# Kernel optimization log

Hardware: AMD Instinct MI355X
Metric: run time of the kernel (lower is better)

## Reference

```python
import jax, jax.numpy as jnp
import numpy as np

B, N, F = 2, 2048, 256
H = 8
O = F // H  # nhid = 32
L = 3       # stacked GraphAttentionLayers
ALPHA = 0.2
NEG = jnp.float32(-1e15)


def setup_inputs() -> dict:
    key = jax.random.key(0)
    ks = jax.random.split(key, 6)
    x = jax.random.normal(ks[0], (B, N, F), dtype=jnp.float32)
    adj = jax.random.randint(ks[1], (B, N, N), 0, 2, dtype=jnp.int32)
    # per-layer multi-head params: W [L,H,F,O], a [L,H,2O]
    W_heads = jax.random.normal(ks[2], (L, H, F, O), dtype=jnp.float32) * 0.1
    a_heads = jax.random.normal(ks[3], (L, H, 2 * O), dtype=jnp.float32) * 0.1
    # per-layer out_att params (single head, F->F)
    W_out = jax.random.normal(ks[4], (L, F, F), dtype=jnp.float32) * 0.05
    a_out = jax.random.normal(ks[5], (L, 2 * F), dtype=jnp.float32) * 0.05
    return {"x": x, "adj": adj, "W_heads": W_heads, "a_heads": a_heads,
            "W_out": W_out, "a_out": a_out}


def _gat_heads(h, mask, W, a1, a2):
    """h: [B,N,F], mask: [B,N,N] bool, W: [H,F,O], a1/a2: [H,O] -> [B,H,N,O]."""
    Wh = jnp.einsum('bnf,hfo->bhno', h, W)
    s1 = jnp.einsum('bhno,ho->bhn', Wh, a1)   # a[:O] projection
    s2 = jnp.einsum('bhno,ho->bhn', Wh, a2)   # a[O:] projection
    e = s1[:, :, :, None] + s2[:, :, None, :]  # additive score [B,H,N,N]
    e = jnp.where(e > 0, e, ALPHA * e)         # LeakyReLU(alpha)
    e = jnp.where(mask[:, None, :, :], e, NEG)
    att = jax.nn.softmax(e, axis=-1)           # dropout is identity in eval
    hp = jnp.einsum('bhnm,bhmo->bhno', att, Wh)
    return jax.nn.elu(hp)                      # activate_function inside head


def reference(x, adj, W_heads, a_heads, W_out, a_out):
    mask = adj > 0
    h = x
    for l in range(L):
        a1 = a_heads[l, :, :O]
        a2 = a_heads[l, :, O:]
        hh = _gat_heads(h, mask, W_heads[l], a1, a2)      # [B,H,N,O]
        h = jnp.transpose(hh, (0, 2, 1, 3)).reshape(B, N, F)  # concat heads
        ao1 = a_out[l, :F][None]
        ao2 = a_out[l, F:][None]
        ho = _gat_heads(h, mask, W_out[l][None], ao1, ao2)[:, 0]  # [B,N,F]
        h = jax.nn.elu(ho)  # extra F.elu in GraphAttentionLayer (elu twice)
    return h
```

## Files before the change

### kernel.cpp

```cpp
#include <hip/hip_runtime.h>
#include <math.h>

#if __has_builtin(__builtin_amdgcn_exp2f)
#define EXP2(x) __builtin_amdgcn_exp2f(x)
#else
#define EXP2(x) exp2f(x)
#endif

#define ALPHA_LRELU 0.2f
#define LOG2E 1.4426950408889634f
#define ESHIFT 6.0f
#define BIGM 1024.0f

constexpr int Bc = 2, Nn = 2048, Ff = 256, Hh = 8, Oo = 32;

typedef _Float16 f16;
typedef f16 f16x8 __attribute__((ext_vector_type(8)));
typedef f16 f16x4 __attribute__((ext_vector_type(4)));
typedef float f32x4 __attribute__((ext_vector_type(4)));
typedef unsigned long long u64;
typedef unsigned u32;

__global__ __launch_bounds__(256) void zero_kernel(float* __restrict__ p) {
    p[blockIdx.x * 256 + threadIdx.x] = 0.f;
}

__global__ __launch_bounds__(256) void pack_kernel(
    const int* __restrict__ adj, u32* __restrict__ maskT) {
    int idx = blockIdx.x * 256 + threadIdx.x;
    u64 bl = __ballot(adj[idx] != 0);
    int lane = threadIdx.x & 63;
    int i = (idx >> 11) & 2047;
    int b = idx >> 22;
    int j0 = (idx & 2047) & ~63;
    int c32 = j0 >> 5;
    if (lane == 0)
        maskT[((size_t)b * 64 + c32) * 2048 + i] = (u32)bl;
    else if (lane == 1)
        maskT[((size_t)b * 64 + c32 + 1) * 2048 + i] = (u32)(bl >> 32);
}

__global__ __launch_bounds__(256) void wt_kernel(
    const float* __restrict__ W_heads, const float* __restrict__ W_out,
    f16* __restrict__ WTF) {
    int t = threadIdx.x;
    int y = blockIdx.y;
    int l = y >> 1, st = y & 1;
    int col = blockIdx.x * 4 + (t >> 6);
    int k0 = (t & 63) * 4;
    const float* src;
    int stride;
    if (st == 0) {
        src = W_heads + (((size_t)l * Hh + (col >> 5)) * Ff) * Oo + (col & 31);
        stride = Oo;
    } else {
        src = W_out + (size_t)l * Ff * Ff + col;
        stride = Ff;
    }
    f16x4 v;
#pragma unroll
    for (int i = 0; i < 4; ++i) v[i] = (f16)src[(size_t)(k0 + i) * stride];
    int cg = col >> 4, am = col & 15;
    int c = k0 >> 5, aq = (k0 >> 3) & 3, i0 = k0 & 7;
    WTF += (((size_t)y * 16 + cg) * 8 + c) * 512 + (aq * 16 + am) * 8 + i0;
    *(f16x4*)WTF = v;
}

__global__ __launch_bounds__(256) void apack_kernel(
    const float* __restrict__ A, f16* __restrict__ Af) {
    int t = threadIdx.x;
    int lane = t & 63;
    int slot = blockIdx.x * 4 + (t >> 6);
    int am = lane & 15, aq = lane >> 4;
    int mt = slot >> 3, c = slot & 7;
    const float* ap = A + ((size_t)mt * 16 + am) * Ff + c * 32 + aq * 8;
    f32x4 v0 = *(const f32x4*)ap;
    f32x4 v1 = *(const f32x4*)(ap + 4);
    f16x8 o;
#pragma unroll
    for (int i = 0; i < 4; ++i) { o[i] = (f16)v0[i]; o[4 + i] = (f16)v1[i]; }
    *(f16x8*)&Af[(size_t)slot * 512 + lane * 8] = o;
}

__global__ __launch_bounds__(256) void gemm_wave(
    const f16* __restrict__ Af, const f16* __restrict__ WTF,
    const float* __restrict__ pa, f16* __restrict__ WhFrag,
    float* __restrict__ s1, float* __restrict__ s2,
    int G, int Ofull, int oshift) {
    int t = threadIdx.x;
    int w = t >> 6, lane = t & 63;
    int am = lane & 15, aq = lane >> 4;
    int mt = blockIdx.x * 4 + w;
    int colb = blockIdx.y * 16;

    const f16* ap = Af + (size_t)(mt * 8) * 512 + lane * 8;
    const f16* bp = WTF + (size_t)((colb >> 4) * 8) * 512 + lane * 8;

    f32x4 acc = {0.f, 0.f, 0.f, 0.f};
    f16x8 a0 = *(const f16x8*)ap;
    f16x8 b0 = *(const f16x8*)bp;
#pragma unroll
    for (int c = 0; c < 8; ++c) {
        int cn = (c + 1 < 8) ? c + 1 : 0;
        f16x8 an = *(const f16x8*)(ap + cn * 512);
        f16x8 bn = *(const f16x8*)(bp + cn * 512);
        acc = __builtin_amdgcn_mfma_f32_16x16x32_f16(a0, b0, acc, 0, 0, 0);
        a0 = an; b0 = bn;
    }

    int m0 = mt * 16;
    int b = m0 >> 11;
    int nn0 = (m0 & 2047) + aq * 4;
    int cO = (m0 & 2047) >> 5;
    int aq_p = ((mt & 1) << 1) | (aq >> 1);
    int i0p = (aq & 1) << 2;
    int g = colb >> oshift;
    size_t bg = (size_t)b * G + g;
    int cg = (colb & (Ofull - 1)) >> 4;

    f16x4 c4;
#pragma unroll
    for (int e = 0; e < 4; ++e) c4[e] = (f16)acc[e];
    *(f16x4*)&WhFrag[(((bg * (Ofull >> 4) + cg) * 64 + cO) * 512) +
                     (aq_p * 16 + am) * 8 + i0p] = c4;

    int o0 = (colb & (Ofull - 1)) + am;
    const float* a1p = pa + 2 * (size_t)g * Ofull;
    float a10 = a1p[o0];
    float a20 = a1p[Ofull + o0];
#pragma unroll
    for (int e = 0; e < 4; ++e) {
        float p1 = acc[e] * a10;
        float p2 = acc[e] * a20;
#pragma unroll
        for (int s = 1; s < 16; s <<= 1) {
            p1 += __shfl_xor(p1, s);
            p2 += __shfl_xor(p2, s);
        }
        if (am == 0) {
            size_t sidx = bg * Nn + nn0 + e;
            atomicAdd(&s1[sidx], p1);
            atomicAdd(&s2[sidx], p2);
        }
    }
}

template <bool OUT, bool FINAL>
__global__ __launch_bounds__(256) void attn_kernel(
    const f16* __restrict__ WhFrag, const float* __restrict__ s1,
    const float* __restrict__ s2, const u32* __restrict__ maskT,
    float* __restrict__ dst, f16* __restrict__ AfOut) {
    constexpr float C0 = -ESHIFT * LOG2E - BIGM;
    constexpr int NCG = OUT ? 16 : 2;
    constexpr int TSTR = 40;
    __shared__ float Ls[4][64];
    __shared__ float As[4][64][8];
    __shared__ f16 T[2][16 * TSTR];

    int t = threadIdx.x;
    int w = t >> 6, lane = t & 63;
    int am = lane & 15, aq = lane >> 4;
    int wr = w & 1;
    int wh = w >> 1;
    int i0 = blockIdx.x * 32 + wr * 16;
    int bz = blockIdx.z;
    int b = OUT ? bz : (bz >> 3);
    int cg0 = OUT ? blockIdx.y * 2 : 0;
    int dstcol = OUT ? cg0 * 16 : (bz & 7) * Oo;

    const f16* bp0 = WhFrag + ((size_t)bz * NCG + cg0) * 64 * 512 + lane * 8;
    const f16* bp1 = bp0 + 64 * 512;
    const float* s2p = s2 + (size_t)bz * Nn + aq * 8;
    float s1v = s1[(size_t)bz * Nn + i0 + am];
    const u32* mtp = maskT + (size_t)b * 64 * 2048 + i0 + am;

    f32x4 acc0 = {0.f, 0.f, 0.f, 0.f}, acc1 = acc0;
    float lacc = 0.f;

    int cbeg = wh * 32, cend = cbeg + 32;

    f16x8 xb0, xb1, yb0, yb1;
    f32x4 xv0, xv1, yv0, yv1;
    u32 xm, ym;
    auto ld = [&](int c, f16x8& b0, f16x8& b1, f32x4& v0, f32x4& v1, u32& m) {
        b0 = *(const f16x8*)(bp0 + c * 512);
        b1 = *(const f16x8*)(bp1 + c * 512);
        v0 = *(const f32x4*)(s2p + c * 32);
        v1 = *(const f32x4*)(s2p + c * 32 + 4);
        m = mtp[c * 2048];
    };
    auto comp = [&](f16x8 b0, f16x8 b1, f32x4 v0, f32x4 v1, u32 m) {
        u32 bits = (m >> (aq * 8)) & 0xffu;
        f16x8 af;
#pragma unroll
        for (int k = 0; k < 8; ++k) {
            float xv = s1v + (k < 4 ? v0[k] : v1[k - 4]);
            float lr = fmaxf(xv, ALPHA_LRELU * xv);
            float bitf = (float)((bits >> k) & 1u);
            float p = EXP2(fmaf(bitf, BIGM, fmaf(lr, LOG2E, C0)));
            lacc += p;
            af[k] = (f16)p;
        }
        acc0 = __builtin_amdgcn_mfma_f32_16x16x32_f16(af, b0, acc0, 0, 0, 0);
        acc1 = __builtin_amdgcn_mfma_f32_16x16x32_f16(af, b1, acc1, 0, 0, 0);
    };

    ld(cbeg, xb0, xb1, xv0, xv1, xm);
    ld(cbeg + 1, yb0, yb1, yv0, yv1, ym);
    for (int c = cbeg; c < cend; c += 2) {
        comp(xb0, xb1, xv0, xv1, xm);
        ld(c + 2 < cend ? c + 2 : cbeg, xb0, xb1, xv0, xv1, xm);
        comp(yb0, yb1, yv0, yv1, ym);
        ld(c + 3 < cend ? c + 3 : cbeg, yb0, yb1, yv0, yv1, ym);
    }

    lacc += __shfl_xor(lacc, 16);
    lacc += __shfl_xor(lacc, 32);

    Ls[w][lane] = lacc;
#pragma unroll
    for (int e = 0; e < 4; ++e) {
        As[w][lane][e] = acc0[e];
        As[w][lane][4 + e] = acc1[e];
    }
    __syncthreads();

    if (wh == 0) {
        float lt = Ls[w][lane] + Ls[w + 2][lane];
        f32x4 a0, a1;
#pragma unroll
        for (int e = 0; e < 4; ++e) {
            a0[e] = As[w][lane][e] + As[w + 2][lane][e];
            a1[e] = As[w][lane][4 + e] + As[w + 2][lane][4 + e];
        }
        f16* Tw = T[wr];
#pragma unroll
        for (int e = 0; e < 4; ++e) {
            int r = aq * 4 + e;
            float li = __shfl(lt, r);
            float v0 = a0[e] / li, v1 = a1[e] / li;
            v0 = v0 > 0.f ? v0 : __expf(v0) - 1.f;
            v1 = v1 > 0.f ? v1 : __expf(v1) - 1.f;
            if (OUT) {
                v0 = v0 > 0.f ? v0 : __expf(v0) - 1.f;
                v1 = v1 > 0.f ? v1 : __expf(v1) - 1.f;
            }
            if (FINAL) {
                size_t base = ((size_t)b * Nn + i0 + r) * Ff + dstcol;
                dst[base + am] = v0;
                dst[base + 16 + am] = v1;
            } else {
                Tw[r * TSTR + am] = (f16)v0;
                Tw[r * TSTR + 16 + am] = (f16)v1;
            }
        }
        if (!FINAL) {
            f16x8 o = *(const f16x8*)&Tw[am * TSTR + aq * 8];
            int mt = (b * Nn + i0) >> 4;
            int c = dstcol >> 5;
            *(f16x8*)&AfOut[(size_t)(mt * 8 + c) * 512 + lane * 8] = o;
        }
    }
}

extern "C" void kernel_launch(void* const* d_in, const int* in_sizes, int n_in,
                              void* d_out, int out_size, void* d_ws, size_t ws_size,
                              hipStream_t stream) {
    const float* x = (const float*)d_in[0];
    const int* adj = (const int*)d_in[1];
    const float* W_heads = (const float*)d_in[2];
    const float* a_heads = (const float*)d_in[3];
    const float* W_out = (const float*)d_in[4];
    const float* a_out = (const float*)d_in[5];
    float* out = (float*)d_out;

    float* ws = (float*)d_ws;
    const size_t M = (size_t)Bc * Nn * Ff;
    f16* Af_a = (f16*)ws;
    f16* Af_b = (f16*)(ws + M / 2);
    f16* WhFrag = (f16*)(ws + M);
    u32* maskT = (u32*)(ws + 3 * M / 2);
    f16* WTF = (f16*)(ws + 3 * M / 2 + M / 4);
    float* sbuf = ws + 3 * M / 2 + M / 4 + 196608;
    const size_t SH = (size_t)Bc * Hh * Nn;
    const size_t SO = (size_t)Bc * Nn;
    const size_t SL = 2 * SH + 2 * SO;

    zero_kernel<<<(3 * SL) / 256, 256, 0, stream>>>(sbuf);
    pack_kernel<<<(Bc * Nn * Nn) / 256, 256, 0, stream>>>(adj, maskT);
    wt_kernel<<<dim3(Ff / 4, 6), 256, 0, stream>>>(W_heads, W_out, WTF);
    apack_kernel<<<(Bc * Nn * Ff / 8) / 256, 256, 0, stream>>>(x, Af_a);

    for (int l = 0; l < 3; ++l) {
        float* s1h = sbuf + l * SL;
        float* s2h = s1h + SH;
        float* s1o = s2h + SH;
        float* s2o = s1o + SO;

        gemm_wave<<<dim3((Bc * Nn) / 64, Ff / 16), 256, 0, stream>>>(
            Af_a, WTF + (size_t)(2 * l) * Ff * Ff,
            a_heads + (size_t)l * Hh * 2 * Oo, WhFrag, s1h, s2h, Hh, Oo, 5);
        attn_kernel<false, false><<<dim3(Nn / 32, 1, Bc * Hh), 256, 0, stream>>>(
            WhFrag, s1h, s2h, maskT, nullptr, Af_b);

        gemm_wave<<<dim3((Bc * Nn) / 64, Ff / 16), 256, 0, stream>>>(
            Af_b, WTF + (size_t)(2 * l + 1) * Ff * Ff,
            a_out + (size_t)l * 2 * Ff, WhFrag, s1o, s2o, 1, Ff, 8);
        if (l == 2) {
            attn_kernel<true, true><<<dim3(Nn / 32, Ff / 32, Bc), 256, 0, stream>>>(
                WhFrag, s1o, s2o, maskT, out, nullptr);
        } else {
            attn_kernel<true, false><<<dim3(Nn / 32, Ff / 32, Bc), 256, 0, stream>>>(
                WhFrag, s1o, s2o, maskT, nullptr, Af_a);
        }
    }
}
```

Before: 301.7 us.

## Fuse all stages into one persistent kernel with hierarchical grid barriers

Replaces the sequence of about sixteen kernel launches (zeroing, packing, GEMMs, attention per layer) with one persistent mega-kernel of 1024 blocks. Stages are separated by a two-level atomic grid barrier, and a small init kernel zeroes the score buffers and barrier counters. The aim is to remove launch overhead and inter-kernel gaps. The risks are deadlock if all 1024 blocks cannot be co-resident (launch_bounds 256,4 is meant to allow this), spin-wait cost at each barrier, and added register pressure in the fused kernel.

```diff
diff --git a/kernel.cpp b/kernel.cpp
--- a/kernel.cpp
+++ b/kernel.cpp
@@ -13,6 +13,7 @@
 #define BIGM 1024.0f
 
 constexpr int Bc = 2, Nn = 2048, Ff = 256, Hh = 8, Oo = 32;
+constexpr int NBLK = 1024;
 
 typedef _Float16 f16;
 typedef f16 f16x8 __attribute__((ext_vector_type(8)));
@@ -21,77 +22,42 @@
 typedef unsigned long long u64;
 typedef unsigned u32;
 
-__global__ __launch_bounds__(256) void zero_kernel(float* __restrict__ p) {
-    p[blockIdx.x * 256 + threadIdx.x] = 0.f;
-}
-
-__global__ __launch_bounds__(256) void pack_kernel(
-    const int* __restrict__ adj, u32* __restrict__ maskT) {
-    int idx = blockIdx.x * 256 + threadIdx.x;
-    u64 bl = __ballot(adj[idx] != 0);
-    int lane = threadIdx.x & 63;
-    int i = (idx >> 11) & 2047;
-    int b = idx >> 22;
-    int j0 = (idx & 2047) & ~63;
-    int c32 = j0 >> 5;
-    if (lane == 0)
-        maskT[((size_t)b * 64 + c32) * 2048 + i] = (u32)bl;
-    else if (lane == 1)
-        maskT[((size_t)b * 64 + c32 + 1) * 2048 + i] = (u32)(bl >> 32);
-}
-
-__global__ __launch_bounds__(256) void wt_kernel(
-    const float* __restrict__ W_heads, const float* __restrict__ W_out,
-    f16* __restrict__ WTF) {
-    int t = threadIdx.x;
-    int y = blockIdx.y;
-    int l = y >> 1, st = y & 1;
-    int col = blockIdx.x * 4 + (t >> 6);
-    int k0 = (t & 63) * 4;
-    const float* src;
-    int stride;
-    if (st == 0) {
-        src = W_heads + (((size_t)l * Hh + (col >> 5)) * Ff) * Oo + (col & 31);
-        stride = Oo;
-    } else {
-        src = W_out + (size_t)l * Ff * Ff + col;
-        stride = Ff;
-    }
-    f16x4 v;
-#pragma unroll
-    for (int i = 0; i < 4; ++i) v[i] = (f16)src[(size_t)(k0 + i) * stride];
-    int cg = col >> 4, am = col & 15;
-    int c = k0 >> 5, aq = (k0 >> 3) & 3, i0 = k0 & 7;
-    WTF += (((size_t)y * 16 + cg) * 8 + c) * 512 + (aq * 16 + am) * 8 + i0;
-    *(f16x4*)WTF = v;
-}
-
-__global__ __launch_bounds__(256) void apack_kernel(
-    const float* __restrict__ A, f16* __restrict__ Af) {
-    int t = threadIdx.x;
-    int lane = t & 63;
-    int slot = blockIdx.x * 4 + (t >> 6);
-    int am = lane & 15, aq = lane >> 4;
-    int mt = slot >> 3, c = slot & 7;
-    const float* ap = A + ((size_t)mt * 16 + am) * Ff + c * 32 + aq * 8;
-    f32x4 v0 = *(const f32x4*)ap;
-    f32x4 v1 = *(const f32x4*)(ap + 4);
-    f16x8 o;
-#pragma unroll
-    for (int i = 0; i < 4; ++i) { o[i] = (f16)v0[i]; o[4 + i] = (f16)v1[i]; }
-    *(f16x8*)&Af[(size_t)slot * 512 + lane * 8] = o;
-}
-
-__global__ __launch_bounds__(256) void gemm_wave(
+__global__ __launch_bounds__(256) void init_kernel(float* __restrict__ sbuf,
+                                                   u32* __restrict__ bar) {
+    int g = blockIdx.x * 256 + threadIdx.x;
+    if (g < 544) bar[g] = 0;
+    if (g < 221184) sbuf[g] = 0.f;
+}
+
+__device__ __forceinline__ void gridbar(u32* bar, int ph) {
+    __syncthreads();
+    if (threadIdx.x == 0) {
+        __threadfence();
+        u32* lv1 = bar + 32 + (blockIdx.x & 15) * 32;
+        u32 old = __hip_atomic_fetch_add(lv1, 1u, __ATOMIC_RELAXED,
+                                         __HIP_MEMORY_SCOPE_AGENT);
+        if (old == (u32)(ph * 64 + 63))
+            __hip_atomic_fetch_add(bar, 1u, __ATOMIC_RELAXED,
+                                   __HIP_MEMORY_SCOPE_AGENT);
+        while (__hip_atomic_load(bar, __ATOMIC_RELAXED,
+                                 __HIP_MEMORY_SCOPE_AGENT) <
+               (u32)(ph * 16 + 16))
+            __builtin_amdgcn_s_sleep(2);
+        __threadfence();
+    }
+    __syncthreads();
+}
+
+__device__ __forceinline__ void gemm_phase(
     const f16* __restrict__ Af, const f16* __restrict__ WTF,
     const float* __restrict__ pa, f16* __restrict__ WhFrag,
     float* __restrict__ s1, float* __restrict__ s2,
-    int G, int Ofull, int oshift) {
+    int G, int Ofull, int oshift, int xb, int yb) {
     int t = threadIdx.x;
     int w = t >> 6, lane = t & 63;
     int am = lane & 15, aq = lane >> 4;
-    int mt = blockIdx.x * 4 + w;
-    int colb = blockIdx.y * 16;
+    int mt = xb * 4 + w;
+    int colb = yb * 16;
 
     const f16* ap = Af + (size_t)(mt * 8) * 512 + lane * 8;
     const f16* bp = WTF + (size_t)((colb >> 4) * 8) * 512 + lane * 8;
@@ -146,26 +112,24 @@
 }
 
 template <bool OUT, bool FINAL>
-__global__ __launch_bounds__(256) void attn_kernel(
+__device__ __forceinline__ void attn_phase(
     const f16* __restrict__ WhFrag, const float* __restrict__ s1,
     const float* __restrict__ s2, const u32* __restrict__ maskT,
-    float* __restrict__ dst, f16* __restrict__ AfOut) {
+    float* __restrict__ dst, f16* __restrict__ AfOut,
+    int xb, int yb, int bz,
+    float (&Ls)[4][64], float (&As)[4][64][8], f16 (&T)[2][640]) {
     constexpr float C0 = -ESHIFT * LOG2E - BIGM;
     constexpr int NCG = OUT ? 16 : 2;
     constexpr int TSTR = 40;
-    __shared__ float Ls[4][64];
-    __shared__ float As[4][64][8];
-    __shared__ f16 T[2][16 * TSTR];
 
     int t = threadIdx.x;
     int w = t >> 6, lane = t & 63;
     int am = lane & 15, aq = lane >> 4;
     int wr = w & 1;
     int wh = w >> 1;
-    int i0 = blockIdx.x * 32 + wr * 16;
-    int bz = blockIdx.z;
+    int i0 = xb * 32 + wr * 16;
     int b = OUT ? bz : (bz >> 3);
-    int cg0 = OUT ? blockIdx.y * 2 : 0;
+    int cg0 = OUT ? yb * 2 : 0;
     int dstcol = OUT ? cg0 * 16 : (bz & 7) * Oo;
 
     const f16* bp0 = WhFrag + ((size_t)bz * NCG + cg0) * 64 * 512 + lane * 8;
@@ -263,6 +227,109 @@
     }
 }
 
+__global__ __launch_bounds__(256, 4) void mega_kernel(
+    const int* __restrict__ adj, const float* __restrict__ x,
+    const float* __restrict__ W_heads, const float* __restrict__ a_heads,
+    const float* __restrict__ W_out, const float* __restrict__ a_out,
+    float* __restrict__ out, f16* __restrict__ Af_a, f16* __restrict__ Af_b,
+    f16* __restrict__ WhFrag, u32* __restrict__ maskT, f16* __restrict__ WTF,
+    float* __restrict__ sbuf, u32* __restrict__ bar) {
+    __shared__ float Ls[4][64];
+    __shared__ float As[4][64][8];
+    __shared__ f16 T[2][640];
+
+    const int B = blockIdx.x;
+    const int t = threadIdx.x;
+    int ph = 0;
+
+    if (B < 768) {
+        for (int idx = B * 256 + t; idx < Bc * Nn * Nn; idx += 768 * 256) {
+            u64 bl = __ballot(adj[idx] != 0);
+            int lane = t & 63;
+            int i = (idx >> 11) & 2047;
+            int b = idx >> 22;
+            int c32 = ((idx & 2047) & ~63) >> 5;
+            if (lane == 0)
+                maskT[((size_t)b * 64 + c32) * 2048 + i] = (u32)bl;
+            else if (lane == 1)
+                maskT[((size_t)b * 64 + c32 + 1) * 2048 + i] = (u32)(bl >> 32);
+        }
+    } else if (B < 896) {
+        int w = t >> 6, lane = t & 63;
+        int am = lane & 15, aq = lane >> 4;
+#pragma unroll
+        for (int it = 0; it < 4; ++it) {
+            int slot = (B - 768) * 4 + w + it * 512;
+            int mt = slot >> 3, c = slot & 7;
+            const float* ap = x + ((size_t)mt * 16 + am) * Ff + c * 32 + aq * 8;
+            f32x4 v0 = *(const f32x4*)ap;
+            f32x4 v1 = *(const f32x4*)(ap + 4);
+            f16x8 o;
+#pragma unroll
+            for (int i = 0; i < 4; ++i) { o[i] = (f16)v0[i]; o[4 + i] = (f16)v1[i]; }
+            *(f16x8*)&Af_a[(size_t)slot * 512 + lane * 8] = o;
+        }
+    } else {
+#pragma unroll
+        for (int it = 0; it < 3; ++it) {
+            int unit = (B - 896) * 3 + it;
+            int y = unit >> 6, bx = unit & 63;
+            int ll = y >> 1, st = y & 1;
+            int col = bx * 4 + (t >> 6);
+            int k0 = (t & 63) * 4;
+            const float* src;
+            int stride;
+            if (st == 0) {
+                src = W_heads + (((size_t)ll * Hh + (col >> 5)) * Ff) * Oo + (col & 31);
+                stride = Oo;
+            } else {
+                src = W_out + (size_t)ll * Ff * Ff + col;
+                stride = Ff;
+            }
+            f16x4 v;
+#pragma unroll
+            for (int i = 0; i < 4; ++i) v[i] = (f16)src[(size_t)(k0 + i) * stride];
+            int cg = col >> 4, am = col & 15;
+            int c = k0 >> 5, aq = (k0 >> 3) & 3, i0 = k0 & 7;
+            *(f16x4*)&WTF[(((size_t)y * 16 + cg) * 8 + c) * 512 +
+                          (aq * 16 + am) * 8 + i0] = v;
+        }
+    }
+    gridbar(bar, ph++);
+
+    const size_t SH = (size_t)Bc * Hh * Nn;
+    const size_t SO = (size_t)Bc * Nn;
+    const size_t SL = 2 * SH + 2 * SO;
+
+    for (int l = 0; l < 3; ++l) {
+        float* s1h = sbuf + l * SL;
+        float* s2h = s1h + SH;
+        float* s1o = s2h + SH;
+        float* s2o = s1o + SO;
+
+        gemm_phase(Af_a, WTF + (size_t)(2 * l) * Ff * Ff,
+                   a_heads + (size_t)l * Hh * 2 * Oo, WhFrag, s1h, s2h,
+                   Hh, Oo, 5, B & 63, B >> 6);
+        gridbar(bar, ph++);
+        attn_phase<false, false>(WhFrag, s1h, s2h, maskT, nullptr, Af_b,
+                                 B & 63, 0, B >> 6, Ls, As, T);
+        gridbar(bar, ph++);
+
+        gemm_phase(Af_b, WTF + (size_t)(2 * l + 1) * Ff * Ff,
+                   a_out + (size_t)l * 2 * Ff, WhFrag, s1o, s2o,
+                   1, Ff, 8, B & 63, B >> 6);
+        gridbar(bar, ph++);
+        if (l == 2) {
+            attn_phase<true, true>(WhFrag, s1o, s2o, maskT, out, nullptr,
+                                   B & 63, (B >> 6) & 7, B >> 9, Ls, As, T);
+        } else {
+            attn_phase<true, false>(WhFrag, s1o, s2o, maskT, nullptr, Af_a,
+                                    B & 63, (B >> 6) & 7, B >> 9, Ls, As, T);
+            gridbar(bar, ph++);
+        }
+    }
+}
+
 extern "C" void kernel_launch(void* const* d_in, const int* in_sizes, int n_in,
                               void* d_out, int out_size, void* d_ws, size_t ws_size,
                               hipStream_t stream) {
@@ -282,36 +349,10 @@
     u32* maskT = (u32*)(ws + 3 * M / 2);
     f16* WTF = (f16*)(ws + 3 * M / 2 + M / 4);
     float* sbuf = ws + 3 * M / 2 + M / 4 + 196608;
-    const size_t SH = (size_t)Bc * Hh * Nn;
-    const size_t SO = (size_t)Bc * Nn;
-    const size_t SL = 2 * SH + 2 * SO;
-
-    zero_kernel<<<(3 * SL) / 256, 256, 0, stream>>>(sbuf);
-    pack_kernel<<<(Bc * Nn * Nn) / 256, 256, 0, stream>>>(adj, maskT);
-    wt_kernel<<<dim3(Ff / 4, 6), 256, 0, stream>>>(W_heads, W_out, WTF);
-    apack_kernel<<<(Bc * Nn * Ff / 8) / 256, 256, 0, stream>>>(x, Af_a);
-
-    for (int l = 0; l < 3; ++l) {
-        float* s1h = sbuf + l * SL;
-        float* s2h = s1h + SH;
-        float* s1o = s2h + SH;
-        float* s2o = s1o + SO;
-
-        gemm_wave<<<dim3((Bc * Nn) / 64, Ff / 16), 256, 0, stream>>>(
-            Af_a, WTF + (size_t)(2 * l) * Ff * Ff,
-            a_heads + (size_t)l * Hh * 2 * Oo, WhFrag, s1h, s2h, Hh, Oo, 5);
-        attn_kernel<false, false><<<dim3(Nn / 32, 1, Bc * Hh), 256, 0, stream>>>(
-            WhFrag, s1h, s2h, maskT, nullptr, Af_b);
-
-        gemm_wave<<<dim3((Bc * Nn) / 64, Ff / 16), 256, 0, stream>>>(
-            Af_b, WTF + (size_t)(2 * l + 1) * Ff * Ff,
-            a_out + (size_t)l * 2 * Ff, WhFrag, s1o, s2o, 1, Ff, 8);
-        if (l == 2) {
-            attn_kernel<true, true><<<dim3(Nn / 32, Ff / 32, Bc), 256, 0, stream>>>(
-                WhFrag, s1o, s2o, maskT, out, nullptr);
-        } else {
-            attn_kernel<true, false><<<dim3(Nn / 32, Ff / 32, Bc), 256, 0, stream>>>(
-                WhFrag, s1o, s2o, maskT, nullptr, Af_a);
-        }
-    }
-}
+    u32* bar = (u32*)(sbuf + 221184);
+
+    init_kernel<<<NBLK, 256, 0, stream>>>(sbuf, bar);
+    mega_kernel<<<NBLK, 256, 0, stream>>>(
+        adj, x, W_heads, a_heads, W_out, a_out, out,
+        Af_a, Af_b, WhFrag, maskT, WTF, sbuf, bar);
+}
```

Measured after the change: 762.5 us. 2.53x slower.

## Merge prep kernels into one launch and give each attention wave two row tiles

Applied to the files above, without the earlier changes.

The four setup kernels (zeroing, mask bit-packing, weight transpose, input packing) become one prep kernel that splits its blocks by role, cutting launch overhead. In the attention kernel each wave now handles both 16-row tiles over a quarter of the column range, so each loaded Wh fragment and s2 vector feeds four MFMAs instead of two. The cross-wave reduction now sums four partials through larger shared arrays. This adds register pressure and shared memory use.

```diff
diff --git a/kernel.cpp b/kernel.cpp
--- a/kernel.cpp
+++ b/kernel.cpp
@@ -21,65 +21,69 @@
 typedef unsigned long long u64;
 typedef unsigned u32;
 
-__global__ __launch_bounds__(256) void zero_kernel(float* __restrict__ p) {
-    p[blockIdx.x * 256 + threadIdx.x] = 0.f;
-}
-
-__global__ __launch_bounds__(256) void pack_kernel(
-    const int* __restrict__ adj, u32* __restrict__ maskT) {
-    int idx = blockIdx.x * 256 + threadIdx.x;
-    u64 bl = __ballot(adj[idx] != 0);
-    int lane = threadIdx.x & 63;
-    int i = (idx >> 11) & 2047;
-    int b = idx >> 22;
-    int j0 = (idx & 2047) & ~63;
-    int c32 = j0 >> 5;
-    if (lane == 0)
-        maskT[((size_t)b * 64 + c32) * 2048 + i] = (u32)bl;
-    else if (lane == 1)
-        maskT[((size_t)b * 64 + c32 + 1) * 2048 + i] = (u32)(bl >> 32);
-}
-
-__global__ __launch_bounds__(256) void wt_kernel(
+__global__ __launch_bounds__(256) void prep_kernel(
+    const int* __restrict__ adj, const float* __restrict__ x,
     const float* __restrict__ W_heads, const float* __restrict__ W_out,
-    f16* __restrict__ WTF) {
-    int t = threadIdx.x;
-    int y = blockIdx.y;
-    int l = y >> 1, st = y & 1;
-    int col = blockIdx.x * 4 + (t >> 6);
-    int k0 = (t & 63) * 4;
-    const float* src;
-    int stride;
-    if (st == 0) {
-        src = W_heads + (((size_t)l * Hh + (col >> 5)) * Ff) * Oo + (col & 31);
-        stride = Oo;
+    u32* __restrict__ maskT, f16* __restrict__ Af, f16* __restrict__ WTF,
+    float* __restrict__ sbuf) {
+    const int B = blockIdx.x;
+    const int t = threadIdx.x;
+    int g = B * 256 + t;
+    if (g < 221184) sbuf[g] = 0.f;
+
+    if (B < 768) {
+        for (int idx = g; idx < Bc * Nn * Nn; idx += 768 * 256) {
+            u64 bl = __ballot(adj[idx] != 0);
+            int lane = t & 63;
+            int i = (idx >> 11) & 2047;
+            int b = idx >> 22;
+            int c32 = ((idx & 2047) & ~63) >> 5;
+            if (lane == 0)
+                maskT[((size_t)b * 64 + c32) * 2048 + i] = (u32)bl;
+            else if (lane == 1)
+                maskT[((size_t)b * 64 + c32 + 1) * 2048 + i] = (u32)(bl >> 32);
+        }
+    } else if (B < 896) {
+        int w = t >> 6, lane = t & 63;
+        int am = lane & 15, aq = lane >> 4;
+#pragma unroll
+        for (int it = 0; it < 4; ++it) {
+            int slot = (B - 768) * 4 + w + it * 512;
+            int mt = slot >> 3, c = slot & 7;
+            const float* ap = x + ((size_t)mt * 16 + am) * Ff + c * 32 + aq * 8;
+            f32x4 v0 = *(const f32x4*)ap;
+            f32x4 v1 = *(const f32x4*)(ap + 4);
+            f16x8 o;
+#pragma unroll
+            for (int i = 0; i < 4; ++i) { o[i] = (f16)v0[i]; o[4 + i] = (f16)v1[i]; }
+            *(f16x8*)&Af[(size_t)slot * 512 + lane * 8] = o;
+        }
     } else {
-        src = W_out + (size_t)l * Ff * Ff + col;
-        stride = Ff;
-    }
-    f16x4 v;
-#pragma unroll
-    for (int i = 0; i < 4; ++i) v[i] = (f16)src[(size_t)(k0 + i) * stride];
-    int cg = col >> 4, am = col & 15;
-    int c = k0 >> 5, aq = (k0 >> 3) & 3, i0 = k0 & 7;
-    WTF += (((size_t)y * 16 + cg) * 8 + c) * 512 + (aq * 16 + am) * 8 + i0;
-    *(f16x4*)WTF = v;
-}
-
-__global__ __launch_bounds__(256) void apack_kernel(
-    const float* __restrict__ A, f16* __restrict__ Af) {
-    int t = threadIdx.x;
-    int lane = t & 63;
-    int slot = blockIdx.x * 4 + (t >> 6);
-    int am = lane & 15, aq = lane >> 4;
-    int mt = slot >> 3, c = slot & 7;
-    const float* ap = A + ((size_t)mt * 16 + am) * Ff + c * 32 + aq * 8;
-    f32x4 v0 = *(const f32x4*)ap;
-    f32x4 v1 = *(const f32x4*)(ap + 4);
-    f16x8 o;
-#pragma unroll
-    for (int i = 0; i < 4; ++i) { o[i] = (f16)v0[i]; o[4 + i] = (f16)v1[i]; }
-    *(f16x8*)&Af[(size_t)slot * 512 + lane * 8] = o;
+#pragma unroll
+        for (int it = 0; it < 3; ++it) {
+            int unit = (B - 896) * 3 + it;
+            int y = unit >> 6, bx = unit & 63;
+            int ll = y >> 1, st = y & 1;
+            int col = bx * 4 + (t >> 6);
+            int k0 = (t & 63) * 4;
+            const float* src;
+            int stride;
+            if (st == 0) {
+                src = W_heads + (((size_t)ll * Hh + (col >> 5)) * Ff) * Oo + (col & 31);
+                stride = Oo;
+            } else {
+                src = W_out + (size_t)ll * Ff * Ff + col;
+                stride = Ff;
+            }
+            f16x4 v;
+#pragma unroll
+            for (int i = 0; i < 4; ++i) v[i] = (f16)src[(size_t)(k0 + i) * stride];
+            int cg = col >> 4, am = col & 15;
+            int c = k0 >> 5, aq = (k0 >> 3) & 3, i0 = k0 & 7;
+            *(f16x4*)&WTF[(((size_t)y * 16 + cg) * 8 + c) * 512 +
+                          (aq * 16 + am) * 8 + i0] = v;
+        }
+    }
 }
 
 __global__ __launch_bounds__(256) void gemm_wave(
@@ -153,16 +157,14 @@
     constexpr float C0 = -ESHIFT * LOG2E - BIGM;
     constexpr int NCG = OUT ? 16 : 2;
     constexpr int TSTR = 40;
-    __shared__ float Ls[4][64];
-    __shared__ float As[4][64][8];
+    __shared__ float Ls[4][2][64];
+    __shared__ float As[4][64][16];
     __shared__ f16 T[2][16 * TSTR];
 
     int t = threadIdx.x;
     int w = t >> 6, lane = t & 63;
     int am = lane & 15, aq = lane >> 4;
-    int wr = w & 1;
-    int wh = w >> 1;
-    int i0 = blockIdx.x * 32 + wr * 16;
+    int i0 = blockIdx.x * 32;
     int bz = blockIdx.z;
     int b = OUT ? bz : (bz >> 3);
     int cg0 = OUT ? blockIdx.y * 2 : 0;
@@ -171,69 +173,90 @@
     const f16* bp0 = WhFrag + ((size_t)bz * NCG + cg0) * 64 * 512 + lane * 8;
     const f16* bp1 = bp0 + 64 * 512;
     const float* s2p = s2 + (size_t)bz * Nn + aq * 8;
-    float s1v = s1[(size_t)bz * Nn + i0 + am];
-    const u32* mtp = maskT + (size_t)b * 64 * 2048 + i0 + am;
-
-    f32x4 acc0 = {0.f, 0.f, 0.f, 0.f}, acc1 = acc0;
-    float lacc = 0.f;
-
-    int cbeg = wh * 32, cend = cbeg + 32;
+    float s1v0 = s1[(size_t)bz * Nn + i0 + am];
+    float s1v1 = s1[(size_t)bz * Nn + i0 + 16 + am];
+    const u32* mtp0 = maskT + (size_t)b * 64 * 2048 + i0 + am;
+    const u32* mtp1 = mtp0 + 16;
+
+    f32x4 acc00 = {0.f, 0.f, 0.f, 0.f}, acc01 = acc00, acc10 = acc00, acc11 = acc00;
+    float lacc0 = 0.f, lacc1 = 0.f;
+
+    int cbeg = w * 16, cend = cbeg + 16;
 
     f16x8 xb0, xb1, yb0, yb1;
     f32x4 xv0, xv1, yv0, yv1;
-    u32 xm, ym;
-    auto ld = [&](int c, f16x8& b0, f16x8& b1, f32x4& v0, f32x4& v1, u32& m) {
+    u32 xm0, xm1, ym0, ym1;
+    auto ld = [&](int c, f16x8& b0, f16x8& b1, f32x4& v0, f32x4& v1,
+                  u32& m0, u32& m1) {
         b0 = *(const f16x8*)(bp0 + c * 512);
         b1 = *(const f16x8*)(bp1 + c * 512);
         v0 = *(const f32x4*)(s2p + c * 32);
         v1 = *(const f32x4*)(s2p + c * 32 + 4);
-        m = mtp[c * 2048];
+        m0 = mtp0[c * 2048];
+        m1 = mtp1[c * 2048];
     };
-    auto comp = [&](f16x8 b0, f16x8 b1, f32x4 v0, f32x4 v1, u32 m) {
-        u32 bits = (m >> (aq * 8)) & 0xffu;
-        f16x8 af;
+    auto comp = [&](f16x8 b0, f16x8 b1, f32x4 v0, f32x4 v1, u32 m0, u32 m1) {
+        u32 bits0 = (m0 >> (aq * 8)) & 0xffu;
+        u32 bits1 = (m1 >> (aq * 8)) & 0xffu;
+        f16x8 af0, af1;
 #pragma unroll
         for (int k = 0; k < 8; ++k) {
-            float xv = s1v + (k < 4 ? v0[k] : v1[k - 4]);
-            float lr = fmaxf(xv, ALPHA_LRELU * xv);
-            float bitf = (float)((bits >> k) & 1u);
-            float p = EXP2(fmaf(bitf, BIGM, fmaf(lr, LOG2E, C0)));
-            lacc += p;
-            af[k] = (f16)p;
-        }
-        acc0 = __builtin_amdgcn_mfma_f32_16x16x32_f16(af, b0, acc0, 0, 0, 0);
-        acc1 = __builtin_amdgcn_mfma_f32_16x16x32_f16(af, b1, acc1, 0, 0, 0);
+            float sv = (k < 4 ? v0[k] : v1[k - 4]);
+            float x0 = s1v0 + sv;
+            float x1 = s1v1 + sv;
+            float lr0 = fmaxf(x0, ALPHA_LRELU * x0);
+            float lr1 = fmaxf(x1, ALPHA_LRELU * x1);
+            float bf0 = (float)((bits0 >> k) & 1u);
+            float bf1 = (float)((bits1 >> k) & 1u);
+            float p0 = EXP2(fmaf(bf0, BIGM, fmaf(lr0, LOG2E, C0)));
+            float p1 = EXP2(fmaf(bf1, BIGM, fmaf(lr1, LOG2E, C0)));
+            lacc0 += p0;
+            lacc1 += p1;
+            af0[k] = (f16)p0;
+            af1[k] = (f16)p1;
+        }
+        acc00 = __builtin_amdgcn_mfma_f32_16x16x32_f16(af0, b0, acc00, 0, 0, 0);
+        acc01 = __builtin_amdgcn_mfma_f32_16x16x32_f16(af0, b1, acc01, 0, 0, 0);
+        acc10 = __builtin_amdgcn_mfma_f32_16x16x32_f16(af1, b0, acc10, 0, 0, 0);
+        acc11 = __builtin_amdgcn_mfma_f32_16x16x32_f16(af1, b1, acc11, 0, 0, 0);
     };
 
-    ld(cbeg, xb0, xb1, xv0, xv1, xm);
-    ld(cbeg + 1, yb0, yb1, yv0, yv1, ym);
+    ld(cbeg, xb0, xb1, xv0, xv1, xm0, xm1);
+    ld(cbeg + 1, yb0, yb1, yv0, yv1, ym0, ym1);
     for (int c = cbeg; c < cend; c += 2) {
-        comp(xb0, xb1, xv0, xv1, xm);
-        ld(c + 2 < cend ? c + 2 : cbeg, xb0, xb1, xv0, xv1, xm);
-        comp(yb0, yb1, yv0, yv1, ym);
-        ld(c + 3 < cend ? c + 3 : cbeg, yb0, yb1, yv0, yv1, ym);
-    }
-
-    lacc += __shfl_xor(lacc, 16);
-    lacc += __shfl_xor(lacc, 32);
-
-    Ls[w][lane] = lacc;
+        comp(xb0, xb1, xv0, xv1, xm0, xm1);
+        ld(c + 2 < cend ? c + 2 : cbeg, xb0, xb1, xv0, xv1, xm0, xm1);
+        comp(yb0, yb1, yv0, yv1, ym0, ym1);
+        ld(c + 3 < cend ? c + 3 : cbeg, yb0, yb1, yv0, yv1, ym0, ym1);
+    }
+
+    lacc0 += __shfl_xor(lacc0, 16);
+    lacc0 += __shfl_xor(lacc0, 32);
+    lacc1 += __shfl_xor(lacc1, 16);
+    lacc1 += __shfl_xor(lacc1, 32);
+
+    Ls[w][0][lane] = lacc0;
+    Ls[w][1][lane] = lacc1;
 #pragma unroll
     for (int e = 0; e < 4; ++e) {
-        As[w][lane][e] = acc0[e];
-        As[w][lane][4 + e] = acc1[e];
+        As[w][lane][e] = acc00[e];
+        As[w][lane][4 + e] = acc01[e];
+        As[w][lane][8 + e] = acc10[e];
+        As[w][lane][12 + e] = acc11[e];
     }
     __syncthreads();
 
-    if (wh == 0) {
-        float lt = Ls[w][lane] + Ls[w + 2][lane];
+    if (w < 2) {
+        float lt = Ls[0][w][lane] + Ls[1][w][lane] + Ls[2][w][lane] + Ls[3][w][lane];
         f32x4 a0, a1;
 #pragma unroll
         for (int e = 0; e < 4; ++e) {
-            a0[e] = As[w][lane][e] + As[w + 2][lane][e];
-            a1[e] = As[w][lane][4 + e] + As[w + 2][lane][4 + e];
-        }
-        f16* Tw = T[wr];
+            a0[e] = As[0][lane][w * 8 + e] + As[1][lane][w * 8 + e] +
+                    As[2][lane][w * 8 + e] + As[3][lane][w * 8 + e];
+            a1[e] = As[0][lane][w * 8 + 4 + e] + As[1][lane][w * 8 + 4 + e] +
+                    As[2][lane][w * 8 + 4 + e] + As[3][lane][w * 8 + 4 + e];
+        }
+        f16* Tw = T[w];
 #pragma unroll
         for (int e = 0; e < 4; ++e) {
             int r = aq * 4 + e;
@@ -246,7 +269,7 @@
                 v1 = v1 > 0.f ? v1 : __expf(v1) - 1.f;
             }
             if (FINAL) {
-                size_t base = ((size_t)b * Nn + i0 + r) * Ff + dstcol;
+                size_t base = ((size_t)b * Nn + i0 + w * 16 + r) * Ff + dstcol;
                 dst[base + am] = v0;
                 dst[base + 16 + am] = v1;
             } else {
@@ -256,7 +279,7 @@
         }
         if (!FINAL) {
             f16x8 o = *(const f16x8*)&Tw[am * TSTR + aq * 8];
-            int mt = (b * Nn + i0) >> 4;
+            int mt = (b * Nn + i0 + w * 16) >> 4;
             int c = dstcol >> 5;
             *(f16x8*)&AfOut[(size_t)(mt * 8 + c) * 512 + lane * 8] = o;
         }
@@ -286,10 +309,8 @@
     const size_t SO = (size_t)Bc * Nn;
     const size_t SL = 2 * SH + 2 * SO;
 
-    zero_kernel<<<(3 * SL) / 256, 256, 0, stream>>>(sbuf);
-    pack_kernel<<<(Bc * Nn * Nn) / 256, 256, 0, stream>>>(adj, maskT);
-    wt_kernel<<<dim3(Ff / 4, 6), 256, 0, stream>>>(W_heads, W_out, WTF);
-    apack_kernel<<<(Bc * Nn * Ff / 8) / 256, 256, 0, stream>>>(x, Af_a);
+    prep_kernel<<<1024, 256, 0, stream>>>(adj, x, W_heads, W_out,
+                                          maskT, Af_a, WTF, sbuf);
 
     for (int l = 0; l < 3; ++l) {
         float* s1h = sbuf + l * SL;
```

Result: faster. 289.7 us (-4.0%).
